# Kernel tuning notes

Measured on AMD Instinct MI355X. Metric: run time of the kernel, lower is better.

Reference implementation:

```python
import jax, jax.numpy as jnp
import numpy as np

N = 100000   # nodes
E = 400000   # edges
G = 5000     # graphs (20 nodes each)
H = 128      # hidden_channels
ATOM_D, BOND_D, BOOL_D = 16, 8, 2
NODE_D = 30 + ATOM_D + 3 * BOOL_D   # 52
EDGE_D = 2 + BOND_D + 3 * BOOL_D    # 16


def setup_inputs() -> dict:
    key = jax.random.key(0)
    ks = jax.random.split(key, 24)
    rn = lambda k, shape: jax.random.normal(k, shape, dtype=jnp.float32) * 0.05
    # node features: [atom_idx, 10 continuous, 3 bools]
    atom_idx = jax.random.randint(ks[0], (N,), 1, 119)
    node_cont = jax.random.normal(ks[1], (N, 10), dtype=jnp.float32)
    node_bool = jax.random.randint(ks[2], (N, 3), 0, 2)
    x = jnp.concatenate([atom_idx[:, None].astype(jnp.float32), node_cont,
                         node_bool.astype(jnp.float32)], axis=1)
    # edge features: [bond_idx, 1 continuous, 3 bools]
    bond_idx = jax.random.randint(ks[3], (E,), 1, 22)
    edge_cont = jax.random.normal(ks[4], (E, 1), dtype=jnp.float32)
    edge_bool = jax.random.randint(ks[5], (E, 3), 0, 2)
    edge_attr = jnp.concatenate([bond_idx[:, None].astype(jnp.float32), edge_cont,
                                 edge_bool.astype(jnp.float32)], axis=1)
    edge_index = jax.random.randint(ks[6], (2, E), 0, N)
    batch = jnp.repeat(jnp.arange(G, dtype=jnp.int32), N // G)
    # embeddings (with padding rows zeroed, as nn.Embedding padding_idx)
    atom_emb = rn(ks[7], (119, ATOM_D)).at[0].set(0.0)
    bond_emb = rn(ks[8], (22, BOND_D)).at[0].set(0.0)
    bool_emb = rn(ks[9], (3, BOOL_D)).at[2].set(0.0)
    Wn = rn(ks[10], (10, 30)); bn = jnp.zeros((30,), jnp.float32)
    We = rn(ks[11], (1, 2));   be = jnp.zeros((2,), jnp.float32)
    Wl1 = rn(ks[12], (NODE_D, H)); bl1 = jnp.zeros((H,), jnp.float32)
    Wr1 = rn(ks[13], (NODE_D, H)); br1 = jnp.zeros((H,), jnp.float32)
    Wedge1 = rn(ks[14], (EDGE_D, H)); att1 = rn(ks[15], (H,))
    bias1 = jnp.zeros((H,), jnp.float32)
    Wl2 = rn(ks[16], (H, H)); bl2 = jnp.zeros((H,), jnp.float32)
    Wr2 = rn(ks[17], (H, H)); br2 = jnp.zeros((H,), jnp.float32)
    Wedge2 = rn(ks[18], (EDGE_D, H)); att2 = rn(ks[19], (H,))
    bias2 = jnp.zeros((H,), jnp.float32)
    return dict(x=x, edge_index=edge_index, edge_attr=edge_attr, batch=batch,
                atom_emb=atom_emb, bond_emb=bond_emb, bool_emb=bool_emb,
                Wn=Wn, bn=bn, We=We, be=be,
                Wl1=Wl1, bl1=bl1, Wr1=Wr1, br1=br1, Wedge1=Wedge1, att1=att1, bias1=bias1,
                Wl2=Wl2, bl2=bl2, Wr2=Wr2, br2=br2, Wedge2=Wedge2, att2=att2, bias2=bias2)


def _gatv2(h, src, dst, e_lin, Wl, bl, Wr, br, att, bias):
    # PyG GATv2Conv, heads=1: xl = lin_l(x) (source), xr = lin_r(x) (target)
    xl = h @ Wl + bl
    xr = h @ Wr + br
    m = xl[src] + xr[dst] + e_lin                      # [E', H]
    a = jax.nn.leaky_relu(m, 0.2) @ att                # [E']
    amax = jax.ops.segment_max(a, dst, num_segments=N)
    ex = jnp.exp(a - amax[dst])
    denom = jax.ops.segment_sum(ex, dst, num_segments=N)
    alpha = ex / denom[dst]                            # softmax over incoming edges
    out = jax.ops.segment_sum(alpha[:, None] * xl[src], dst, num_segments=N)
    return out + bias


def reference(x, edge_index, edge_attr, batch,
              atom_emb, bond_emb, bool_emb, Wn, bn, We, be,
              Wl1, bl1, Wr1, br1, Wedge1, att1, bias1,
              Wl2, bl2, Wr2, br2, Wedge2, att2, bias2):
    # --- encode nodes ---
    ai = x[:, 0].astype(jnp.int32)
    nb = x[:, 11:14].astype(jnp.int32)
    h = jnp.concatenate([atom_emb[ai], x[:, 1:11] @ Wn + bn,
                         bool_emb[nb[:, 0]], bool_emb[nb[:, 1]], bool_emb[nb[:, 2]]], axis=1)
    # --- encode edges ---
    bi = edge_attr[:, 0].astype(jnp.int32)
    eb = edge_attr[:, 2:5].astype(jnp.int32)
    e = jnp.concatenate([bond_emb[bi], edge_attr[:, 1:2] @ We + be,
                         bool_emb[eb[:, 0]], bool_emb[eb[:, 1]], bool_emb[eb[:, 2]]], axis=1)
    src, dst = edge_index[0], edge_index[1]
    # --- add self loops with fill_value='mean' (mean of in-edge attrs per node) ---
    cnt = jax.ops.segment_sum(jnp.ones((E,), h.dtype), dst, num_segments=N)
    loop_attr = jax.ops.segment_sum(e, dst, num_segments=N) / jnp.maximum(cnt, 1.0)[:, None]
    e_full = jnp.concatenate([e, loop_attr], axis=0)          # [E+N, EDGE_D]
    loop = jnp.arange(N, dtype=src.dtype)
    src_f = jnp.concatenate([src, loop])
    dst_f = jnp.concatenate([dst, loop])
    # --- 3 GATv2 layers (layers 2 and 3 share weights, as in the original) ---
    h = jax.nn.relu(_gatv2(h, src_f, dst_f, e_full @ Wedge1, Wl1, bl1, Wr1, br1, att1, bias1))
    e_lin2 = e_full @ Wedge2
    h = jax.nn.relu(_gatv2(h, src_f, dst_f, e_lin2, Wl2, bl2, Wr2, br2, att2, bias2))
    h = jax.nn.relu(_gatv2(h, src_f, dst_f, e_lin2, Wl2, bl2, Wr2, br2, att2, bias2))
    # --- global_max_pool readout ---
    return jax.ops.segment_max(h, batch, num_segments=G)
```

## Files before the change

### kernel.cpp

```cpp
#include <hip/hip_runtime.h>
#include <hip/hip_fp16.h>

#define N_NODES 100000
#define N_EDGES 400000
#define N_GRAPHS 5000
#define NPG 20
#define SCAN_NB 256
#define SCAN_CHUNK ((N_NODES + SCAN_NB - 1) / SCAN_NB)
#define TAB_STRIDE (256 * 128 + 128)
#define F1 8192
#define F2 16384
#define NB_ENC ((N_NODES + 255) / 256)
#define NB_HIST ((N_EDGES + 255) / 256)

typedef __attribute__((ext_vector_type(8))) _Float16 f16x8;
typedef __attribute__((ext_vector_type(2))) _Float16 h2;
typedef __attribute__((ext_vector_type(4))) float f32x4;

__global__ __launch_bounds__(256) void k_prologue(
    const float* __restrict__ x, const float* __restrict__ atom_emb,
    const float* __restrict__ bool_emb, const float* __restrict__ Wn,
    const float* __restrict__ bn, __half* __restrict__ h0,
    const int* __restrict__ dst, int* __restrict__ cnt,
    const float* __restrict__ Wedge1, const float* __restrict__ Wedge2,
    const float* __restrict__ bond_emb, const float* __restrict__ We,
    const float* __restrict__ be, __half* __restrict__ tabs,
    const float* __restrict__ Wl1, const float* __restrict__ Wr1,
    const float* __restrict__ Wl2, const float* __restrict__ Wr2,
    unsigned short* __restrict__ fr) {
  int b = blockIdx.x, tid = threadIdx.x;
  if (b < NB_ENC) {
    int n = b * 256 + tid;
    if (n >= N_NODES) return;
    const float* xr = x + (size_t)n * 14;
    __half* h = h0 + (size_t)n * 64;
    int ai = (int)xr[0];
    #pragma unroll
    for (int j = 0; j < 16; j++) h[j] = __float2half(atom_emb[ai * 16 + j]);
    float xc[10];
    #pragma unroll
    for (int k = 0; k < 10; k++) xc[k] = xr[1 + k];
    #pragma unroll
    for (int c = 0; c < 30; c++) {
      float s = bn[c];
      #pragma unroll
      for (int k = 0; k < 10; k++) s += xc[k] * Wn[k * 30 + c];
      h[16 + c] = __float2half(s);
    }
    #pragma unroll
    for (int t = 0; t < 3; t++) {
      int bb = (int)xr[11 + t];
      h[46 + 2 * t]     = __float2half(bool_emb[2 * bb]);
      h[46 + 2 * t + 1] = __float2half(bool_emb[2 * bb + 1]);
    }
    #pragma unroll
    for (int j = 52; j < 64; j++) h[j] = __float2half(0.0f);
  } else if (b < NB_ENC + NB_HIST) {
    int e = (b - NB_ENC) * 256 + tid;
    if (e >= N_EDGES) return;
    atomicAdd(cnt + dst[e], 1);
  } else if (b == NB_ENC + NB_HIST) {
    int s = tid >> 7, c = tid & 127;
    const float* W = s ? Wedge2 : Wedge1;
    __half* T12 = tabs + (size_t)s * TAB_STRIDE;
    __half* v   = T12 + 256 * 128;
    float w8 = W[8 * 128 + c], w9 = W[9 * 128 + c];
    v[c] = __float2half(We[0] * w8 + We[1] * w9);
    float cst = be[0] * w8 + be[1] * w9;
    float bond[22];
    for (int bb = 0; bb < 22; bb++) {
      float acc = 0.f;
      #pragma unroll
      for (int k = 0; k < 8; k++) acc += bond_emb[bb * 8 + k] * W[k * 128 + c];
      bond[bb] = acc;
    }
    for (int combo = 0; combo < 8; combo++) {
      float t2 = cst;
      #pragma unroll
      for (int tt = 0; tt < 3; tt++) {
        int bt = (combo >> tt) & 1;
        t2 += bool_emb[bt * 2 + 0] * W[(10 + 2 * tt + 0) * 128 + c];
        t2 += bool_emb[bt * 2 + 1] * W[(10 + 2 * tt + 1) * 128 + c];
      }
      for (int bb = 0; bb < 22; bb++)
        T12[(combo * 32 + bb) * 128 + c] = __float2half(bond[bb] + t2);
      for (int bb = 22; bb < 32; bb++)
        T12[(combo * 32 + bb) * 128 + c] = __float2half(0.f);
    }
  } else {
    int g = (b - (NB_ENC + NB_HIST + 1)) * 256 + tid;
    const float* W; int K; unsigned short* base; int fl;
    if (g < 1024)      { W = Wl1; K = 52;  base = fr;               fl = g; }
    else if (g < 2048) { W = Wr1; K = 52;  base = fr + F1;          fl = g - 1024; }
    else if (g < 4096) { W = Wl2; K = 128; base = fr + 2 * F1;      fl = g - 2048; }
    else if (g < 6144) { W = Wr2; K = 128; base = fr + 2 * F1 + F2; fl = g - 4096; }
    else return;
    int l = fl & 63, ctn = fl >> 6;
    int tn = ctn & 7, c = ctn >> 3;
    int n = tn * 16 + (l & 15);
    int kb = c * 32 + (l >> 4) * 8;
    unsigned h8[8];
    #pragma unroll
    for (int j = 0; j < 8; j++) {
      int k = kb + j;
      float v = (k < K) ? W[(size_t)k * 128 + n] : 0.f;
      __half hv = __float2half(v);
      h8[j] = (unsigned)*(unsigned short*)&hv;
    }
    uint4 hv4 = make_uint4(h8[0] | (h8[1] << 16), h8[2] | (h8[3] << 16),
                           h8[4] | (h8[5] << 16), h8[6] | (h8[7] << 16));
    *(uint4*)(base + (size_t)fl * 8) = hv4;
  }
}

__global__ __launch_bounds__(256) void k_scan1(const int* __restrict__ cnt,
                                               int* __restrict__ bsum) {
  __shared__ int red[256];
  int b = blockIdx.x, t = threadIdx.x;
  int beg = b * SCAN_CHUNK;
  int end = beg + SCAN_CHUNK; if (end > N_NODES) end = N_NODES;
  int s = 0;
  for (int i = beg + t; i < end; i += 256) s += cnt[i] + 1;
  red[t] = s;
  __syncthreads();
  for (int off = 128; off > 0; off >>= 1) {
    if (t < off) red[t] += red[t + off];
    __syncthreads();
  }
  if (t == 0) bsum[b] = red[0];
}

__global__ __launch_bounds__(256) void k_scan2(int* __restrict__ bsum) {
  __shared__ int sh[256];
  int t = threadIdx.x;
  sh[t] = bsum[t];
  __syncthreads();
  for (int off = 1; off < 256; off <<= 1) {
    int v = (t >= off) ? sh[t - off] : 0;
    __syncthreads();
    sh[t] += v;
    __syncthreads();
  }
  bsum[t] = (t > 0) ? sh[t - 1] : 0;
}

__global__ __launch_bounds__(256) void k_scan3(const int* __restrict__ cnt,
                                               const int* __restrict__ bsum,
                                               int* __restrict__ indptr,
                                               int* __restrict__ cursor) {
  __shared__ int sh[256];
  __shared__ int carry;
  int b = blockIdx.x, t = threadIdx.x;
  int beg = b * SCAN_CHUNK;
  int end = beg + SCAN_CHUNK; if (end > N_NODES) end = N_NODES;
  if (t == 0) carry = bsum[b];
  __syncthreads();
  for (int base = beg; base < end; base += 256) {
    int i = base + t;
    int v = (i < end) ? cnt[i] + 1 : 0;
    sh[t] = v;
    __syncthreads();
    for (int off = 1; off < 256; off <<= 1) {
      int u = (t >= off) ? sh[t - off] : 0;
      __syncthreads();
      sh[t] += u;
      __syncthreads();
    }
    int excl = sh[t] - v;
    if (i < end) {
      int val = carry + excl;
      indptr[i] = val;
      cursor[i] = val;
    }
    __syncthreads();
    if (t == 255) carry += sh[255];
    __syncthreads();
  }
  if (b == 0 && t == 0) indptr[N_NODES] = N_EDGES + N_NODES;
}

__global__ void k_fill(const int* __restrict__ srcA,
                       const int* __restrict__ dst,
                       const float* __restrict__ eattr,
                       int* __restrict__ cursor,
                       int4* __restrict__ scode) {
  int e = blockIdx.x * blockDim.x + threadIdx.x;
  if (e >= N_EDGES) return;
  const float* r = eattr + (size_t)e * 5;
  int bi = (int)r[0];
  float ec = r[1];
  int combo = (int)r[2] + 2 * (int)r[3] + 4 * (int)r[4];
  int meta = bi | (combo << 5);
  int d = dst[e];
  int p = atomicAdd(&cursor[d], 1);
  scode[p] = make_int4(srcA[e], meta, __float_as_int(ec), 0);
}

template <int KPAD>
__global__ __launch_bounds__(256, 4) void k_gemm2m(const __half* __restrict__ A,
                                                   const unsigned short* __restrict__ WfL,
                                                   const unsigned short* __restrict__ WfR,
                                                   const float* __restrict__ bl_,
                                                   const float* __restrict__ br_,
                                                   __half* __restrict__ outl,
                                                   __half* __restrict__ outr) {
  __shared__ unsigned short Bs[2][4096];
  const int tid = threadIdx.x;
  const int wv = tid >> 6, lane = tid & 63;
  const int tw = blockIdx.x * 4 + wv;
  const bool active = (tw < N_NODES / 16);
  const int ml = lane & 15, q = lane >> 4;
  const int m0 = active ? tw * 16 : 0;
  f32x4 accL[8], accR[8];
  #pragma unroll
  for (int t = 0; t < 8; t++) {
    accL[t] = (f32x4){0.f, 0.f, 0.f, 0.f};
    accR[t] = (f32x4){0.f, 0.f, 0.f, 0.f};
  }
  const _Float16* ar0 = (const _Float16*)A + (size_t)(m0 + ml) * KPAD + q * 8;
  constexpr int NC = KPAD / 32;
  for (int c = 0; c < NC; c++) {
    #pragma unroll
    for (int i0 = 0; i0 < 512; i0 += 256) {
      int i = i0 + tid;
      size_t g = ((size_t)c * 512 + i) * 8;
      *(uint4*)(&Bs[0][i * 8]) = *(const uint4*)(WfL + g);
      *(uint4*)(&Bs[1][i * 8]) = *(const uint4*)(WfR + g);
    }
    __syncthreads();
    f16x8 a = *(const f16x8*)(ar0 + c * 32);
    #pragma unroll
    for (int t = 0; t < 8; t++) {
      int idx = (t * 64 + lane) * 8;
      f16x8 bL = *(const f16x8*)(&Bs[0][idx]);
      f16x8 bR = *(const f16x8*)(&Bs[1][idx]);
      accL[t] = __builtin_amdgcn_mfma_f32_16x16x32_f16(a, bL, accL[t], 0, 0, 0);
      accR[t] = __builtin_amdgcn_mfma_f32_16x16x32_f16(a, bR, accR[t], 0, 0, 0);
    }
    __syncthreads();
  }
  if (!active) return;
  #pragma unroll
  for (int t = 0; t < 8; t++) {
    int n = t * 16 + ml;
    float bL = bl_[n], bR = br_[n];
    #pragma unroll
    for (int r = 0; r < 4; r++) {
      int row = m0 + q * 4 + r;
      outl[(size_t)row * 128 + n] = __float2half(accL[t][r] + bL);
      outr[(size_t)row * 128 + n] = __float2half(accR[t][r] + bR);
    }
  }
}

__global__ __launch_bounds__(256) void k_gat(const __half* __restrict__ xl,
                                             const __half* __restrict__ xr,
                                             const int* __restrict__ indptr,
                                             const int4* __restrict__ scode,
                                             const __half* __restrict__ tabs,
                                             const float* __restrict__ att,
                                             const float* __restrict__ bias,
                                             __half* __restrict__ hout) {
  int wid = (blockIdx.x * 256 + threadIdx.x) >> 6;
  int nw = (gridDim.x * 256) >> 6;
  int lane = threadIdx.x & 63;
  int q4 = lane >> 4;
  int c = (lane & 15) * 8;
  const __half* T12 = tabs;
  uint4 vu = *(const uint4*)(tabs + 256 * 128 + c);
  h2 v4[4] = {*reinterpret_cast<h2*>(&vu.x), *reinterpret_cast<h2*>(&vu.y),
              *reinterpret_cast<h2*>(&vu.z), *reinterpret_cast<h2*>(&vu.w)};
  float4 af0 = *(const float4*)(att + c);
  float4 af1 = *(const float4*)(att + c + 4);
  h2 a4[4] = {{(_Float16)af0.x, (_Float16)af0.y}, {(_Float16)af0.z, (_Float16)af0.w},
              {(_Float16)af1.x, (_Float16)af1.y}, {(_Float16)af1.z, (_Float16)af1.w}};
  float bb[8];
  {
    float4 b0 = *(const float4*)(bias + c);
    float4 b1 = *(const float4*)(bias + c + 4);
    bb[0] = b0.x; bb[1] = b0.y; bb[2] = b0.z; bb[3] = b0.w;
    bb[4] = b1.x; bb[5] = b1.y; bb[6] = b1.z; bb[7] = b1.w;
  }
  const h2 z2 = {(_Float16)0.f, (_Float16)0.f};
  const h2 k2 = {(_Float16)0.2f, (_Float16)0.2f};
  wid = __builtin_amdgcn_readfirstlane(wid);
  for (int nb = wid * 4; nb < N_NODES; nb += nw * 4) {
    int n = nb + q4;
    int beg = indptr[n], end1 = indptr[n + 1] - 1;
    int last = (end1 > beg) ? end1 - 1 : beg;
    uint4 xru = *(const uint4*)(xr + (size_t)n * 128 + c);
    h2 xrv[4] = {*reinterpret_cast<h2*>(&xru.x), *reinterpret_cast<h2*>(&xru.y),
                 *reinterpret_cast<h2*>(&xru.z), *reinterpret_cast<h2*>(&xru.w)};
    float denom = 0.f;
    float acc[8] = {0.f, 0.f, 0.f, 0.f, 0.f, 0.f, 0.f, 0.f};
    h2 els[4] = {z2, z2, z2, z2};
    int my_it = (end1 - beg + 3) >> 2;
    int m1 = my_it, m2;
    m2 = __shfl_xor(m1, 16, 64); m1 = m1 > m2 ? m1 : m2;
    m2 = __shfl_xor(m1, 32, 64); m1 = m1 > m2 ? m1 : m2;
    int iters = m1;
    for (int it = 0; it < iters; it++) {
      int j = beg + it * 4;
      int4 sc4[4]; h2 xlv[4][4]; float tt[4];
      bool val[4];
      #pragma unroll
      for (int u = 0; u < 4; u++) {
        val[u] = (j + u < end1);
        int jj = val[u] ? j + u : last;
        sc4[u] = scode[jj];
      }
      #pragma unroll
      for (int u = 0; u < 4; u++) {
        int s = val[u] ? sc4[u].x : n;
        uint4 lv = *(const uint4*)(xl + (size_t)s * 128 + c);
        xlv[u][0] = *reinterpret_cast<h2*>(&lv.x);
        xlv[u][1] = *reinterpret_cast<h2*>(&lv.y);
        xlv[u][2] = *reinterpret_cast<h2*>(&lv.z);
        xlv[u][3] = *reinterpret_cast<h2*>(&lv.w);
      }
      #pragma unroll
      for (int u = 0; u < 4; u++) {
        int meta = val[u] ? (sc4[u].y & 255) : 255;
        float ec = val[u] ? __int_as_float(sc4[u].z) : 0.f;
        uint4 tv = *(const uint4*)(T12 + (size_t)meta * 128 + c);
        h2 t4[4] = {*reinterpret_cast<h2*>(&tv.x), *reinterpret_cast<h2*>(&tv.y),
                    *reinterpret_cast<h2*>(&tv.z), *reinterpret_cast<h2*>(&tv.w)};
        _Float16 eh = (_Float16)ec;
        h2 eh2 = {eh, eh};
        h2 d = z2;
        #pragma unroll
        for (int k = 0; k < 4; k++) {
          h2 el = eh2 * v4[k] + t4[k];
          h2 m = xlv[u][k] + xrv[k] + el;
          h2 l = __builtin_elementwise_max(m, z2) + k2 * __builtin_elementwise_min(m, z2);
          d += l * a4[k];
          els[k] += el;
        }
        tt[u] = (float)d[0] + (float)d[1];
      }
      #pragma unroll
      for (int off = 1; off < 16; off <<= 1) {
        tt[0] += __shfl_xor(tt[0], off, 64);
        tt[1] += __shfl_xor(tt[1], off, 64);
        tt[2] += __shfl_xor(tt[2], off, 64);
        tt[3] += __shfl_xor(tt[3], off, 64);
      }
      #pragma unroll
      for (int u = 0; u < 4; u++) {
        float ex = val[u] ? __expf(tt[u]) : 0.f;
        denom += ex;
        #pragma unroll
        for (int k = 0; k < 4; k++) {
          acc[2 * k]     += ex * (float)xlv[u][k][0];
          acc[2 * k + 1] += ex * (float)xlv[u][k][1];
        }
      }
    }
    int cntn = end1 - beg;
    float inv_cnt = 1.0f / (float)(cntn > 0 ? cntn : 1);
    uint4 xnu = *(const uint4*)(xl + (size_t)n * 128 + c);
    h2 xn[4] = {*reinterpret_cast<h2*>(&xnu.x), *reinterpret_cast<h2*>(&xnu.y),
                *reinterpret_cast<h2*>(&xnu.z), *reinterpret_cast<h2*>(&xnu.w)};
    float afv[8] = {af0.x, af0.y, af0.z, af0.w, af1.x, af1.y, af1.z, af1.w};
    float ts = 0.f;
    float xnf[8];
    #pragma unroll
    for (int k = 0; k < 4; k++) {
      #pragma unroll
      for (int hh = 0; hh < 2; hh++) {
        int i = 2 * k + hh;
        xnf[i] = (float)xn[k][hh];
        float m = xnf[i] + (float)xrv[k][hh] + (float)els[k][hh] * inv_cnt;
        float l = m > 0.f ? m : 0.2f * m;
        ts += l * afv[i];
      }
    }
    #pragma unroll
    for (int off = 1; off < 16; off <<= 1) ts += __shfl_xor(ts, off, 64);
    float ex = __expf(ts);
    denom += ex;
    #pragma unroll
    for (int i = 0; i < 8; i++) acc[i] += ex * xnf[i];
    float invd = 1.0f / denom;
    h2 p[4];
    #pragma unroll
    for (int k = 0; k < 4; k++) {
      float o0 = acc[2 * k] * invd + bb[2 * k];
      float o1 = acc[2 * k + 1] * invd + bb[2 * k + 1];
      o0 = o0 > 0.f ? o0 : 0.f;
      o1 = o1 > 0.f ? o1 : 0.f;
      p[k] = (h2){(_Float16)o0, (_Float16)o1};
    }
    uint4 st = make_uint4(*reinterpret_cast<unsigned*>(&p[0]),
                          *reinterpret_cast<unsigned*>(&p[1]),
                          *reinterpret_cast<unsigned*>(&p[2]),
                          *reinterpret_cast<unsigned*>(&p[3]));
    *(uint4*)(hout + (size_t)n * 128 + c) = st;
  }
}

__global__ void k_readout(const __half* __restrict__ h, float* __restrict__ out) {
  int wid = (blockIdx.x * blockDim.x + threadIdx.x) >> 6;
  int lane = threadIdx.x & 63;
  if (wid >= N_GRAPHS) return;
  int c = lane * 2;
  float m0 = -1e30f, m1 = -1e30f;
  for (int i = 0; i < NPG; i++) {
    unsigned v = *(const unsigned*)(h + ((size_t)(wid * NPG + i)) * 128 + c);
    h2 f = *reinterpret_cast<h2*>(&v);
    m0 = fmaxf(m0, (float)f[0]);
    m1 = fmaxf(m1, (float)f[1]);
  }
  float2 o; o.x = m0; o.y = m1;
  *(float2*)(out + (size_t)wid * 128 + c) = o;
}

extern "C" void kernel_launch(void* const* d_in, const int* in_sizes, int n_in,
                              void* d_out, int out_size, void* d_ws, size_t ws_size,
                              hipStream_t stream) {
  (void)in_sizes; (void)n_in; (void)out_size; (void)ws_size;
  const float* x        = (const float*)d_in[0];
  const int*   eindex   = (const int*)d_in[1];
  const float* eattr    = (const float*)d_in[2];
  const float* atom_emb = (const float*)d_in[4];
  const float* bond_emb = (const float*)d_in[5];
  const float* bool_emb = (const float*)d_in[6];
  const float* Wn   = (const float*)d_in[7];
  const float* bn   = (const float*)d_in[8];
  const float* We   = (const float*)d_in[9];
  const float* be   = (const float*)d_in[10];
  const float* Wl1  = (const float*)d_in[11];
  const float* bl1  = (const float*)d_in[12];
  const float* Wr1  = (const float*)d_in[13];
  const float* br1  = (const float*)d_in[14];
  const float* Wedge1 = (const float*)d_in[15];
  const float* att1 = (const float*)d_in[16];
  const float* bias1 = (const float*)d_in[17];
  const float* Wl2  = (const float*)d_in[18];
  const float* bl2  = (const float*)d_in[19];
  const float* Wr2  = (const float*)d_in[20];
  const float* br2  = (const float*)d_in[21];
  const float* Wedge2 = (const float*)d_in[22];
  const float* att2 = (const float*)d_in[23];
  const float* bias2 = (const float*)d_in[24];

  const int* srcA = eindex;
  const int* dstA = eindex + N_EDGES;

  char* p = (char*)d_ws;
  auto alloc = [&](size_t bytes) {
    char* r = p;
    p += (bytes + 255) & ~(size_t)255;
    return r;
  };
  __half* h0     = (__half*)alloc((size_t)N_NODES * 64 * 2);
  __half* h      = (__half*)alloc((size_t)N_NODES * 128 * 2);
  __half* xl     = (__half*)alloc((size_t)N_NODES * 128 * 2);
  __half* xrb    = (__half*)alloc((size_t)N_NODES * 128 * 2);
  int*    cnt    = (int*)alloc((size_t)N_NODES * 4);
  int*    indptr = (int*)alloc((size_t)(N_NODES + 1) * 4);
  int*    cursor = (int*)alloc((size_t)N_NODES * 4);
  int4*   scode  = (int4*)alloc((size_t)(N_EDGES + N_NODES) * 16);
  __half* tabs   = (__half*)alloc((size_t)2 * TAB_STRIDE * 2);
  unsigned short* wfrag = (unsigned short*)alloc((size_t)(2 * F1 + 2 * F2) * 2);
  int*    bsum   = (int*)alloc((size_t)SCAN_NB * 4);

  (void)hipMemsetAsync(cnt, 0, (size_t)N_NODES * 4, stream);

  k_prologue<<<NB_ENC + NB_HIST + 1 + 24, 256, 0, stream>>>(
      x, atom_emb, bool_emb, Wn, bn, h0, dstA, cnt,
      Wedge1, Wedge2, bond_emb, We, be, tabs,
      Wl1, Wr1, Wl2, Wr2, wfrag);
  k_scan1<<<SCAN_NB, 256, 0, stream>>>(cnt, bsum);
  k_scan2<<<1, 256, 0, stream>>>(bsum);
  k_scan3<<<SCAN_NB, 256, 0, stream>>>(cnt, bsum, indptr, cursor);
  k_fill<<<(N_EDGES + 255) / 256, 256, 0, stream>>>(srcA, dstA, eattr, cursor, scode);

  const unsigned short* f_l1 = wfrag;
  const unsigned short* f_r1 = wfrag + F1;
  const unsigned short* f_l2 = wfrag + 2 * F1;
  const unsigned short* f_r2 = wfrag + 2 * F1 + F2;

  const int GB2 = (N_NODES / 16 + 3) / 4;

  k_gemm2m<64><<<GB2, 256, 0, stream>>>(h0, f_l1, f_r1, bl1, br1, xl, xrb);
  k_gat<<<2048, 256, 0, stream>>>(xl, xrb, indptr, scode, tabs, att1, bias1, h);

  k_gemm2m<128><<<GB2, 256, 0, stream>>>(h, f_l2, f_r2, bl2, br2, xl, xrb);
  k_gat<<<2048, 256, 0, stream>>>(xl, xrb, indptr, scode, tabs + TAB_STRIDE, att2, bias2, h);

  k_gemm2m<128><<<GB2, 256, 0, stream>>>(h, f_l2, f_r2, bl2, br2, xl, xrb);
  k_gat<<<2048, 256, 0, stream>>>(xl, xrb, indptr, scode, tabs + TAB_STRIDE, att2, bias2, h);

  k_readout<<<(N_GRAPHS * 64 + 255) / 256, 256, 0, stream>>>(h, (float*)d_out);
}
```

Before: 351.2 us.

## Stage GEMM output through LDS for coalesced stores, double K-chunk, resize GAT grid

The dual-output GEMM now loads 64-wide K chunks of weight fragments per barrier pair, which halves the number of synchronisations. Its epilogue writes the fp16 results into per-wave LDS scratch and then stores full 16-byte rows to global memory, replacing scattered 2-byte stores. The GAT launch grid changes from a fixed 2048 blocks to a size derived from node count. This doubles LDS use to 32 KB per block, which may reduce occupancy, and the grid change alters how work is spread across waves.

```diff
diff --git a/kernel.cpp b/kernel.cpp
--- a/kernel.cpp
+++ b/kernel.cpp
@@ -204,7 +204,7 @@
                                                    const float* __restrict__ br_,
                                                    __half* __restrict__ outl,
                                                    __half* __restrict__ outr) {
-  __shared__ unsigned short Bs[2][4096];
+  __shared__ unsigned short Bs[2][8192];
   const int tid = threadIdx.x;
   const int wv = tid >> 6, lane = tid & 63;
   const int tw = blockIdx.x * 4 + wv;
@@ -218,38 +218,61 @@
     accR[t] = (f32x4){0.f, 0.f, 0.f, 0.f};
   }
   const _Float16* ar0 = (const _Float16*)A + (size_t)(m0 + ml) * KPAD + q * 8;
-  constexpr int NC = KPAD / 32;
-  for (int c = 0; c < NC; c++) {
-    #pragma unroll
-    for (int i0 = 0; i0 < 512; i0 += 256) {
+  constexpr int NC2 = KPAD / 64;
+  for (int c2 = 0; c2 < NC2; c2++) {
+    #pragma unroll
+    for (int i0 = 0; i0 < 1024; i0 += 256) {
       int i = i0 + tid;
-      size_t g = ((size_t)c * 512 + i) * 8;
+      size_t g = ((size_t)c2 * 1024 + i) * 8;
       *(uint4*)(&Bs[0][i * 8]) = *(const uint4*)(WfL + g);
       *(uint4*)(&Bs[1][i * 8]) = *(const uint4*)(WfR + g);
     }
     __syncthreads();
-    f16x8 a = *(const f16x8*)(ar0 + c * 32);
-    #pragma unroll
-    for (int t = 0; t < 8; t++) {
-      int idx = (t * 64 + lane) * 8;
-      f16x8 bL = *(const f16x8*)(&Bs[0][idx]);
-      f16x8 bR = *(const f16x8*)(&Bs[1][idx]);
-      accL[t] = __builtin_amdgcn_mfma_f32_16x16x32_f16(a, bL, accL[t], 0, 0, 0);
-      accR[t] = __builtin_amdgcn_mfma_f32_16x16x32_f16(a, bR, accR[t], 0, 0, 0);
-    }
-    __syncthreads();
-  }
+    #pragma unroll
+    for (int sub = 0; sub < 2; sub++) {
+      f16x8 a = *(const f16x8*)(ar0 + c2 * 64 + sub * 32);
+      #pragma unroll
+      for (int t = 0; t < 8; t++) {
+        int idx = (sub * 512 + t * 64 + lane) * 8;
+        f16x8 bL = *(const f16x8*)(&Bs[0][idx]);
+        f16x8 bR = *(const f16x8*)(&Bs[1][idx]);
+        accL[t] = __builtin_amdgcn_mfma_f32_16x16x32_f16(a, bL, accL[t], 0, 0, 0);
+        accR[t] = __builtin_amdgcn_mfma_f32_16x16x32_f16(a, bR, accR[t], 0, 0, 0);
+      }
+    }
+    __syncthreads();
+  }
+  __syncthreads();
   if (!active) return;
+  __half* eb = (__half*)&Bs[0][0] + wv * 2048;
+  const int srow = q * 4;
+  const int rrow0 = lane >> 4;
+  const int rcol = (lane & 15) * 8;
   #pragma unroll
   for (int t = 0; t < 8; t++) {
     int n = t * 16 + ml;
-    float bL = bl_[n], bR = br_[n];
-    #pragma unroll
-    for (int r = 0; r < 4; r++) {
-      int row = m0 + q * 4 + r;
-      outl[(size_t)row * 128 + n] = __float2half(accL[t][r] + bL);
-      outr[(size_t)row * 128 + n] = __float2half(accR[t][r] + bR);
-    }
+    float bL = bl_[n];
+    #pragma unroll
+    for (int r = 0; r < 4; r++)
+      eb[(srow + r) * 128 + n] = __float2half(accL[t][r] + bL);
+  }
+  #pragma unroll
+  for (int pp = 0; pp < 4; pp++) {
+    uint4 v = *(const uint4*)(eb + pp * 512 + lane * 8);
+    *(uint4*)(outl + (size_t)(m0 + pp * 4 + rrow0) * 128 + rcol) = v;
+  }
+  #pragma unroll
+  for (int t = 0; t < 8; t++) {
+    int n = t * 16 + ml;
+    float bR = br_[n];
+    #pragma unroll
+    for (int r = 0; r < 4; r++)
+      eb[(srow + r) * 128 + n] = __float2half(accR[t][r] + bR);
+  }
+  #pragma unroll
+  for (int pp = 0; pp < 4; pp++) {
+    uint4 v = *(const uint4*)(eb + pp * 512 + lane * 8);
+    *(uint4*)(outr + (size_t)(m0 + pp * 4 + rrow0) * 128 + rcol) = v;
   }
 }
 
@@ -482,15 +505,16 @@
   const unsigned short* f_r2 = wfrag + 2 * F1 + F2;
 
   const int GB2 = (N_NODES / 16 + 3) / 4;
+  const int GGAT = (N_NODES / 16 + 15) / 16 * 4;
 
   k_gemm2m<64><<<GB2, 256, 0, stream>>>(h0, f_l1, f_r1, bl1, br1, xl, xrb);
-  k_gat<<<2048, 256, 0, stream>>>(xl, xrb, indptr, scode, tabs, att1, bias1, h);
+  k_gat<<<GGAT, 256, 0, stream>>>(xl, xrb, indptr, scode, tabs, att1, bias1, h);
 
   k_gemm2m<128><<<GB2, 256, 0, stream>>>(h, f_l2, f_r2, bl2, br2, xl, xrb);
-  k_gat<<<2048, 256, 0, stream>>>(xl, xrb, indptr, scode, tabs + TAB_STRIDE, att2, bias2, h);
+  k_gat<<<GGAT, 256, 0, stream>>>(xl, xrb, indptr, scode, tabs + TAB_STRIDE, att2, bias2, h);
 
   k_gemm2m<128><<<GB2, 256, 0, stream>>>(h, f_l2, f_r2, bl2, br2, xl, xrb);
-  k_gat<<<2048, 256, 0, stream>>>(xl, xrb, indptr, scode, tabs + TAB_STRIDE, att2, bias2, h);
+  k_gat<<<GGAT, 256, 0, stream>>>(xl, xrb, indptr, scode, tabs + TAB_STRIDE, att2, bias2, h);
 
   k_readout<<<(N_GRAPHS * 64 + 255) / 256, 256, 0, stream>>>(h, (float*)d_out);
 }
```

Measured after the change: 360.5 us. +2.7%, slower.
